# Kernel tuning notes

Measured on AMD Instinct MI355X. Metric: run time of the kernel, lower is better.

Reference implementation:

```python
import jax, jax.numpy as jnp
import numpy as np

N_HEAD = 16
HEAD_DIM = 64
EPS_RMS = 1e-6


def _rope(x, cos, sin):
    # x: [B, T, H, D]; cos/sin: [T, D//2] broadcast to [1, T, 1, D//2]
    d2 = x.shape[-1] // 2
    x1, x2 = x[..., :d2], x[..., d2:]
    c = cos[None, :, None, :]
    s = sin[None, :, None, :]
    return jnp.concatenate([x1 * c + x2 * s, -x1 * s + x2 * c], axis=-1)


def _rms_norm(x):
    return x * jax.lax.rsqrt(jnp.mean(x * x, axis=-1, keepdims=True) + EPS_RMS)


def setup_inputs() -> dict:
    key = jax.random.key(0)
    ks = jax.random.split(key, 7)
    B, T, C = 1, 4096, 1024
    x = jax.random.normal(ks[0], (B, T, C), dtype=jnp.float32)
    # realistic rotary angles
    d2 = HEAD_DIM // 2
    inv_freq = 1.0 / (10000.0 ** (np.arange(0, d2, dtype=np.float32) / d2))
    ang = np.arange(T, dtype=np.float32)[:, None] * inv_freq[None, :]
    cos = jnp.asarray(np.cos(ang), dtype=jnp.float32)
    sin = jnp.asarray(np.sin(ang), dtype=jnp.float32)
    scale = 0.02
    wq = jax.random.normal(ks[1], (C, C), dtype=jnp.float32) * scale
    wk = jax.random.normal(ks[2], (C, C), dtype=jnp.float32) * scale
    wv = jax.random.normal(ks[3], (C, C), dtype=jnp.float32) * scale
    wproj = jax.random.normal(ks[4], (C, C), dtype=jnp.float32) * scale
    return {"x": x, "cos": cos, "sin": sin, "wq": wq, "wk": wk, "wv": wv, "wproj": wproj}


def reference(x, cos, sin, wq, wk, wv, wproj):
    B, T, C = x.shape
    H, D = N_HEAD, HEAD_DIM
    # QKV projections (torch Linear: x @ W.T)
    q = (x @ wq.T).reshape(B, T, H, D)
    k = (x @ wk.T).reshape(B, T, H, D)
    v = (x @ wv.T).reshape(B, T, H, D)
    # RoPE then QK RMS-norm
    q = _rms_norm(_rope(q, cos, sin))
    k = _rms_norm(_rope(k, cos, sin))
    # [B, H, T, D]
    q = q.transpose(0, 2, 1, 3)
    k = k.transpose(0, 2, 1, 3)
    v = v.transpose(0, 2, 1, 3)
    scores = jnp.einsum('bhqd,bhkd->bhqk', q, k) * (1.0 / D ** 0.5)
    # causal mask (kv_cache is None, Tq == Tk == T)
    mask = jnp.tril(jnp.ones((T, T), dtype=bool))
    scores = jnp.where(mask[None, None, :, :], scores, -jnp.inf)
    attn = jax.nn.sigmoid(scores)  # sigmoid(-inf) == 0
    y = jnp.einsum('bhqk,bhkd->bhqd', attn, v)
    y = y / (T ** 0.5 + 1e-6)
    y = y.transpose(0, 2, 1, 3).reshape(B, T, C)
    return y @ wproj.T
```

## Files before the change

kernel.cpp:

```cpp
#include <hip/hip_runtime.h>

typedef __attribute__((ext_vector_type(8))) short bf16x8;
typedef __attribute__((ext_vector_type(4))) float f32x4;
typedef __attribute__((ext_vector_type(16))) float f32x16;

__device__ inline f32x4 mfma16(bf16x8 a, bf16x8 b, f32x4 c) {
    return __builtin_amdgcn_mfma_f32_16x16x32_bf16(a, b, c, 0, 0, 0);
}
__device__ inline f32x16 mfma32(bf16x8 a, bf16x8 b, f32x16 c) {
    return __builtin_amdgcn_mfma_f32_32x32x16_bf16(a, b, c, 0, 0, 0);
}

__device__ inline short f2bf(float f) {
    unsigned u = __builtin_bit_cast(unsigned, f);
    unsigned r = (u + 0x7fffu + ((u >> 16) & 1u)) >> 16;
    return (short)r;
}
__device__ inline float bf2f(short h) {
    unsigned u = ((unsigned)(unsigned short)h) << 16;
    return __builtin_bit_cast(float, u);
}

__device__ inline unsigned cvt_pk_bf16(float lo, float hi) {
    unsigned r;
    asm("v_cvt_pk_bf16_f32 %0, %1, %2" : "=v"(r) : "v"(lo), "v"(hi));
    return r;
}
__device__ inline void plane_swap(unsigned& a, unsigned& b) {
    asm("v_permlane32_swap_b32 %0, %1" : "+v"(a), "+v"(b));
}
__device__ inline float exp2_hw(float x) {
    float r;
    asm("v_exp_f32 %0, %1" : "=v"(r) : "v"(x));
    return r;
}

#define GAS(p) (const __attribute__((address_space(1))) void*)(p)
#define LAS(p) (__attribute__((address_space(3))) void*)(p)

#define T_SEQ 4096
#define C_DIM 1024
#define N_HEAD 16
#define HEAD_DIM 64
#define QSCALE (-0.18033688011112042f)

__global__ __launch_bounds__(256) void cast5(
    const float* __restrict__ s0, const float* __restrict__ s1,
    const float* __restrict__ s2, const float* __restrict__ s3,
    const float* __restrict__ s4,
    short* __restrict__ d0, short* __restrict__ d1, short* __restrict__ d2,
    short* __restrict__ d3, short* __restrict__ d4,
    int n0, int n1, int n2, int n3, int n4)
{
    int z = blockIdx.y;
    const float* s; short* d; int n;
    switch (z) {
        case 0: s = s0; d = d0; n = n0; break;
        case 1: s = s1; d = d1; n = n1; break;
        case 2: s = s2; d = d2; n = n2; break;
        case 3: s = s3; d = d3; n = n3; break;
        default: s = s4; d = d4; n = n4; break;
    }
    int i = (blockIdx.x * 256 + threadIdx.x) * 4;
    if (i >= n) return;
    float4 v = *(const float4*)&s[i];
    short4 o;
    o.x = f2bf(v.x); o.y = f2bf(v.y); o.z = f2bf(v.z); o.w = f2bf(v.w);
    *(short4*)&d[i] = o;
}

template<int OBF>
__global__ __launch_bounds__(256) void gemm3(
    const short* __restrict__ A,
    const short* __restrict__ B0, const short* __restrict__ B1,
    const short* __restrict__ B2,
    void* C0, void* C1, void* C2,
    int M, int N, int K)
{
    const short* B = (blockIdx.z == 0) ? B0 : ((blockIdx.z == 1) ? B1 : B2);
    void*        C = (blockIdx.z == 0) ? C0 : ((blockIdx.z == 1) ? C1 : C2);

    __shared__ alignas(16) short sA[128 * 32];
    __shared__ alignas(16) short sB[128 * 32];

    int tid  = threadIdx.x;
    int wave = tid >> 6, lane = tid & 63;
    int lhi  = lane >> 4, llo = lane & 15;
    int wr   = wave >> 1, wc = wave & 1;
    int row0 = blockIdx.x * 128, col0 = blockIdx.y * 128;

    int srow = lane >> 2;
    int scol = (lane & 3) * 8;

    f32x4 acc[4][4];
#pragma unroll
    for (int m = 0; m < 4; m++)
#pragma unroll
        for (int n = 0; n < 4; n++)
            acc[m][n] = (f32x4){0.f, 0.f, 0.f, 0.f};

    for (int k0 = 0; k0 < K; k0 += 32) {
        __syncthreads();
#pragma unroll
        for (int s2 = 0; s2 < 2; s2++) {
            int rbase = wave * 32 + s2 * 16;
            __builtin_amdgcn_global_load_lds(
                GAS(&A[(size_t)(row0 + rbase + srow) * K + k0 + scol]),
                LAS(&sA[rbase * 32]), 16, 0, 0);
            __builtin_amdgcn_global_load_lds(
                GAS(&B[(size_t)(col0 + rbase + srow) * K + k0 + scol]),
                LAS(&sB[rbase * 32]), 16, 0, 0);
        }
        __syncthreads();

        bf16x8 af[4], bfv[4];
#pragma unroll
        for (int m = 0; m < 4; m++)
            af[m] = *(const bf16x8*)&sA[(wr * 64 + m * 16 + llo) * 32 + lhi * 8];
#pragma unroll
        for (int n = 0; n < 4; n++)
            bfv[n] = *(const bf16x8*)&sB[(wc * 64 + n * 16 + llo) * 32 + lhi * 8];
#pragma unroll
        for (int m = 0; m < 4; m++)
#pragma unroll
            for (int n = 0; n < 4; n++)
                acc[m][n] = mfma16(af[m], bfv[n], acc[m][n]);
    }

#pragma unroll
    for (int m = 0; m < 4; m++)
#pragma unroll
        for (int n = 0; n < 4; n++)
#pragma unroll
            for (int r = 0; r < 4; r++) {
                int row = row0 + wr * 64 + m * 16 + lhi * 4 + r;
                int col = col0 + wc * 64 + n * 16 + llo;
                float v = acc[m][n][r];
                if (OBF) ((short*)C)[(size_t)row * N + col] = f2bf(v);
                else     ((float*)C)[(size_t)row * N + col] = v;
            }
}

__global__ __launch_bounds__(256) void rope_rms(
    const short* __restrict__ Qb, const float* __restrict__ cosT,
    const float* __restrict__ sinT, short* __restrict__ qn, float outscale)
{
    int idx = blockIdx.x * 4 + (threadIdx.x >> 6);
    int t = idx >> 4, h = idx & 15;
    int d = threadIdx.x & 63;

    float v = bf2f(Qb[t * C_DIM + h * HEAD_DIM + d]);
    int d2 = d & 31;
    float c = cosT[t * 32 + d2], s = sinT[t * 32 + d2];
    float other = __shfl_xor(v, 32);
    float r = (d < 32) ? (v * c + other * s) : (v * c - other * s);

    float sq = r * r;
#pragma unroll
    for (int off = 32; off >= 1; off >>= 1) sq += __shfl_xor(sq, off);
    float inv = rsqrtf(sq * (1.0f / 64.0f) + 1e-6f);

    qn[((size_t)h * T_SEQ + t) * HEAD_DIM + d] = f2bf(r * inv * outscale);
}

__global__ __launch_bounds__(256) void vtrans(
    const short* __restrict__ Vb, short* __restrict__ vt)
{
    __shared__ short sT[64 * 65];
    int h = blockIdx.y, tb = blockIdx.x;
    int tid = threadIdx.x;
    const float inv64 = 1.0f / (64.0f + 1e-6f);
#pragma unroll
    for (int i = 0; i < 16; i++) {
        int linear = i * 256 + tid;
        int r = linear >> 6, c = linear & 63;
        float v = bf2f(Vb[(size_t)(tb * 64 + r) * C_DIM + h * HEAD_DIM + c]) * inv64;
        sT[c * 65 + r] = f2bf(v);
    }
    __syncthreads();
#pragma unroll
    for (int i = 0; i < 16; i++) {
        int linear = i * 256 + tid;
        int dd = linear >> 6, tt = linear & 63;
        vt[((size_t)(h * HEAD_DIM + dd)) * T_SEQ + tb * 64 + tt] = sT[dd * 65 + tt];
    }
}


#define STAGE(s_, bf_) do {                                                      \
    int kb_ = (s_) * 64;                                                         \
    int r0_ = wv * 8 + (lane >> 3);                                              \
    int ss_ = (lane & 7) ^ (lane >> 3);                                          \
    __builtin_amdgcn_global_load_lds(                                            \
        GAS(Kh + (size_t)(kb_ + r0_) * HEAD_DIM + ss_ * 8),                      \
        LAS(Smem + (bf_) * 8192 + wv * 1024), 16, 0, 0);                         \
    __builtin_amdgcn_global_load_lds(                                            \
        GAS(Vh + (size_t)r0_ * T_SEQ + kb_ + ss_ * 8),                           \
        LAS(Smem + 16384 + (bf_) * 8192 + wv * 1024), 16, 0, 0);                 \
} while (0)

__global__ __launch_bounds__(512, 4) void attn5(
    const short* __restrict__ qn, const short* __restrict__ kn,
    const short* __restrict__ vt, short* __restrict__ yb)
{
    __shared__ alignas(16) char Smem[32768];

    int id  = blockIdx.x;
    int idx = id >> 3;
    int h   = (id & 7) * 2 + (idx & 1);
    int sq  = idx >> 1;
    int t   = (sq < 16) ? (31 - sq) : (sq - 16);
    int ns  = 2 * t + 2;

    int tid = threadIdx.x, wv = tid >> 6, lane = tid & 63;
    int lo = lane & 31, hi = lane >> 5;
    int band = wv & 3, tm = wv >> 2;

    const short* Qh = qn + (size_t)h * T_SEQ * HEAD_DIM;
    const short* Kh = kn + (size_t)h * T_SEQ * HEAD_DIM;
    const short* Vh = vt + (size_t)h * HEAD_DIM * T_SEQ;

    int q0 = t * 128;
    int qrow  = q0 + band * 32 + lo;
    int qmaxw = q0 + band * 32 + 31;

    const short* Qr = &Qh[(size_t)qrow * HEAD_DIM + hi * 8];
    bf16x8 qf0 = *(const bf16x8*)&Qr[0];
    bf16x8 qf1 = *(const bf16x8*)&Qr[16];
    bf16x8 qf2 = *(const bf16x8*)&Qr[32];
    bf16x8 qf3 = *(const bf16x8*)&Qr[48];

    f32x16 yac0, yac1;
#pragma unroll
    for (int r = 0; r < 16; r++) { yac0[r] = 0.f; yac1[r] = 0.f; }

    unsigned swz   = (unsigned)((lo & 7) << 4);
    unsigned krow  = (unsigned)((tm * 32 + lo) * 128);
    unsigned vbase = 16384u;

    STAGE(0, 0);
    int buf = 0;
    for (int s = 0; s < ns; s++) {
        if (s + 1 < ns) {
            STAGE(s + 1, buf ^ 1);
            asm volatile("s_waitcnt vmcnt(2)" ::: "memory");
        } else {
            asm volatile("s_waitcnt vmcnt(0)" ::: "memory");
        }
        __builtin_amdgcn_s_barrier();

        int kb0 = s * 64 + tm * 32;
        if (kb0 <= qmaxw) {
            const char* KB = Smem + buf * 8192;
            const char* VB = Smem + vbase + buf * 8192;
            bf16x8 kf0 = *(const bf16x8*)(KB + krow + ((0u * 32 + hi * 16) ^ swz));
            bf16x8 kf1 = *(const bf16x8*)(KB + krow + ((1u * 32 + hi * 16) ^ swz));
            bf16x8 kf2 = *(const bf16x8*)(KB + krow + ((2u * 32 + hi * 16) ^ swz));
            bf16x8 kf3 = *(const bf16x8*)(KB + krow + ((3u * 32 + hi * 16) ^ swz));
            unsigned v0r = (unsigned)((0 * 32 + lo) * 128);
            unsigned v1r = (unsigned)((1 * 32 + lo) * 128);
            unsigned vswz = (unsigned)((lo & 7) << 4);
            bf16x8 vf00 = *(const bf16x8*)(VB + v0r + (((unsigned)(tm * 64 + 0 * 32 + hi * 16)) ^ vswz));
            bf16x8 vf01 = *(const bf16x8*)(VB + v0r + (((unsigned)(tm * 64 + 1 * 32 + hi * 16)) ^ vswz));
            bf16x8 vf10 = *(const bf16x8*)(VB + v1r + (((unsigned)(tm * 64 + 0 * 32 + hi * 16)) ^ vswz));
            bf16x8 vf11 = *(const bf16x8*)(VB + v1r + (((unsigned)(tm * 64 + 1 * 32 + hi * 16)) ^ vswz));

            f32x16 sv;
#pragma unroll
            for (int r = 0; r < 16; r++) sv[r] = 0.f;
            __builtin_amdgcn_s_setprio(1);
            sv = mfma32(kf0, qf0, sv);
            sv = mfma32(kf1, qf1, sv);
            sv = mfma32(kf2, qf2, sv);
            sv = mfma32(kf3, qf3, sv);
            __builtin_amdgcn_s_setprio(0);

            if (kb0 + 31 > q0 + band * 32) {
#pragma unroll
                for (int r = 0; r < 16; r++) {
                    int kvg = kb0 + (r & 3) + 8 * (r >> 2) + 4 * hi;
                    float pv = __builtin_amdgcn_rcpf(1.f + exp2_hw(sv[r]));
                    sv[r] = (kvg <= qrow) ? pv : 0.f;
                }
            } else {
#pragma unroll
                for (int r = 0; r < 16; r++)
                    sv[r] = __builtin_amdgcn_rcpf(1.f + exp2_hw(sv[r]));
            }

#pragma unroll
            for (int k2 = 0; k2 < 2; k2++) {
                unsigned wA = cvt_pk_bf16(sv[8 * k2 + 0], sv[8 * k2 + 1]);
                unsigned wC = cvt_pk_bf16(sv[8 * k2 + 2], sv[8 * k2 + 3]);
                unsigned wB = cvt_pk_bf16(sv[8 * k2 + 4], sv[8 * k2 + 5]);
                unsigned wD = cvt_pk_bf16(sv[8 * k2 + 6], sv[8 * k2 + 7]);
                plane_swap(wA, wB);
                plane_swap(wC, wD);
                union { unsigned u[4]; bf16x8 v; } pw;
                pw.u[0] = wA; pw.u[1] = wC; pw.u[2] = wB; pw.u[3] = wD;
                __builtin_amdgcn_s_setprio(1);
                yac0 = mfma32(pw.v, k2 ? vf01 : vf00, yac0);
                yac1 = mfma32(pw.v, k2 ? vf11 : vf10, yac1);
                __builtin_amdgcn_s_setprio(0);
            }
        }
        asm volatile("" ::: "memory");
        __builtin_amdgcn_s_barrier();
        buf ^= 1;
    }

    __syncthreads();
    float* Yred = (float*)Smem;
    if (tm == 1) {
#pragma unroll
        for (int d = 0; d < 2; d++)
#pragma unroll
            for (int r = 0; r < 16; r++) {
                int crow = (r & 3) + 8 * (r >> 2) + 4 * hi;
                Yred[(band * 32 + crow) * 64 + d * 32 + lo] = d ? yac1[r] : yac0[r];
            }
    }
    __syncthreads();
    if (tm == 0) {
#pragma unroll
        for (int d = 0; d < 2; d++)
#pragma unroll
            for (int r = 0; r < 16; r++) {
                int crow = (r & 3) + 8 * (r >> 2) + 4 * hi;
                float v = (d ? yac1[r] : yac0[r]) + Yred[(band * 32 + crow) * 64 + d * 32 + lo];
                yb[(size_t)(q0 + band * 32 + crow) * C_DIM + h * HEAD_DIM + d * 32 + lo] = f2bf(v);
            }
    }
}

extern "C" void kernel_launch(void* const* d_in, const int* in_sizes, int n_in,
                              void* d_out, int out_size, void* d_ws, size_t ws_size,
                              hipStream_t stream)
{
    const float* x    = (const float*)d_in[0];
    const float* cosT = (const float*)d_in[1];
    const float* sinT = (const float*)d_in[2];
    const float* wq   = (const float*)d_in[3];
    const float* wk   = (const float*)d_in[4];
    const float* wv   = (const float*)d_in[5];
    const float* wp   = (const float*)d_in[6];

    char* ws = (char*)d_ws;
    const size_t MB = 1024 * 1024;
    short* xb  = (short*)(ws + 0);
    short* wqb = (short*)(ws + 8  * MB);
    short* wkb = (short*)(ws + 10 * MB);
    short* wvb = (short*)(ws + 12 * MB);
    short* wpb = (short*)(ws + 14 * MB);
    short* Qb  = (short*)(ws + 16 * MB);
    short* Kb  = (short*)(ws + 24 * MB);
    short* Vb  = (short*)(ws + 32 * MB);
    short* qnb = (short*)(ws + 40 * MB);
    short* knb = (short*)(ws + 48 * MB);
    short* vtb = (short*)(ws + 56 * MB);
    short* yb  = (short*)(ws + 64 * MB);

    cast5<<<dim3(4096, 5, 1), 256, 0, stream>>>(
        x, wq, wk, wv, wp, xb, wqb, wkb, wvb, wpb,
        T_SEQ * C_DIM, C_DIM * C_DIM, C_DIM * C_DIM, C_DIM * C_DIM, C_DIM * C_DIM);

    gemm3<1><<<dim3(32, 8, 3), 256, 0, stream>>>(
        xb, wqb, wkb, wvb, (void*)Qb, (void*)Kb, (void*)Vb, T_SEQ, C_DIM, C_DIM);

    rope_rms<<<16384, 256, 0, stream>>>(Qb, cosT, sinT, qnb, QSCALE);
    rope_rms<<<16384, 256, 0, stream>>>(Kb, cosT, sinT, knb, 1.0f);

    vtrans<<<dim3(64, 16, 1), 256, 0, stream>>>(Vb, vtb);

    attn5<<<512, 512, 0, stream>>>(qnb, knb, vtb, yb);

    gemm3<0><<<dim3(32, 8, 1), 256, 0, stream>>>(
        yb, wpb, wpb, wpb, d_out, d_out, d_out, T_SEQ, C_DIM, C_DIM);
}
```

Baseline: 159.4 us.

## Fuse Q/K rope-norm into vectorized kernel and halve attention query tile

The two per-element rope_rms launches become one rope2 kernel that handles both Q and K. Each thread in it processes 8 contiguous bf16 values with vector loads and stores and reduces over an 8-lane shuffle group. The attention kernel moves from 128-query blocks of 8 waves to 64-query blocks of 4 waves, doubling the grid to 1024 blocks with a reordered causal schedule for load balance. Each wave now issues four LDS-direct loads per stage, and LDS offsets are precomputed outside the loop. The aim is to cut launch overhead and narrow memory traffic for rope, and to improve occupancy and balance in attention, at the cost of reloading K/V per query block more often.

```diff
diff --git a/kernel.cpp b/kernel.cpp
--- a/kernel.cpp
+++ b/kernel.cpp
@@ -141,26 +141,54 @@
             }
 }
 
-__global__ __launch_bounds__(256) void rope_rms(
-    const short* __restrict__ Qb, const float* __restrict__ cosT,
-    const float* __restrict__ sinT, short* __restrict__ qn, float outscale)
-{
-    int idx = blockIdx.x * 4 + (threadIdx.x >> 6);
-    int t = idx >> 4, h = idx & 15;
-    int d = threadIdx.x & 63;
-
-    float v = bf2f(Qb[t * C_DIM + h * HEAD_DIM + d]);
-    int d2 = d & 31;
-    float c = cosT[t * 32 + d2], s = sinT[t * 32 + d2];
-    float other = __shfl_xor(v, 32);
-    float r = (d < 32) ? (v * c + other * s) : (v * c - other * s);
-
-    float sq = r * r;
-#pragma unroll
-    for (int off = 32; off >= 1; off >>= 1) sq += __shfl_xor(sq, off);
-    float inv = rsqrtf(sq * (1.0f / 64.0f) + 1e-6f);
-
-    qn[((size_t)h * T_SEQ + t) * HEAD_DIM + d] = f2bf(r * inv * outscale);
+__global__ __launch_bounds__(256) void rope2(
+    const short* __restrict__ Qb, const short* __restrict__ Kb,
+    const float* __restrict__ cosT, const float* __restrict__ sinT,
+    short* __restrict__ qnb, short* __restrict__ knb)
+{
+    int z = blockIdx.y;
+    const short* src = z ? Kb : Qb;
+    short* dst = z ? knb : qnb;
+    float osc = z ? 1.0f : QSCALE;
+
+    int rowg = blockIdx.x * 32 + (threadIdx.x >> 3);
+    int t = rowg >> 4, h = rowg & 15;
+    int j = threadIdx.x & 7;
+
+    bf16x8 v8 = *(const bf16x8*)&src[(size_t)t * C_DIM + h * HEAD_DIM + j * 8];
+    float f[8], o[8];
+#pragma unroll
+    for (int i = 0; i < 8; i++) f[i] = bf2f(v8[i]);
+#pragma unroll
+    for (int i = 0; i < 8; i++) o[i] = __shfl_xor(f[i], 4);
+
+    const float* cp = &cosT[t * 32 + (j & 3) * 8];
+    const float* sp = &sinT[t * 32 + (j & 3) * 8];
+    float4 c0 = *(const float4*)&cp[0], c1 = *(const float4*)&cp[4];
+    float4 s0 = *(const float4*)&sp[0], s1 = *(const float4*)&sp[4];
+    float cc[8] = {c0.x, c0.y, c0.z, c0.w, c1.x, c1.y, c1.z, c1.w};
+    float ss[8] = {s0.x, s0.y, s0.z, s0.w, s1.x, s1.y, s1.z, s1.w};
+
+    float r[8];
+    if (j < 4) {
+#pragma unroll
+        for (int i = 0; i < 8; i++) r[i] = f[i] * cc[i] + o[i] * ss[i];
+    } else {
+#pragma unroll
+        for (int i = 0; i < 8; i++) r[i] = f[i] * cc[i] - o[i] * ss[i];
+    }
+
+    float sq = 0.f;
+#pragma unroll
+    for (int i = 0; i < 8; i++) sq += r[i] * r[i];
+#pragma unroll
+    for (int off = 1; off <= 4; off <<= 1) sq += __shfl_xor(sq, off);
+    float inv = rsqrtf(sq * (1.0f / 64.0f) + 1e-6f) * osc;
+
+    bf16x8 out;
+#pragma unroll
+    for (int i = 0; i < 8; i++) out[i] = f2bf(r[i] * inv);
+    *(bf16x8*)&dst[((size_t)h * T_SEQ + t) * HEAD_DIM + j * 8] = out;
 }
 
 __global__ __launch_bounds__(256) void vtrans(
@@ -187,40 +215,46 @@
 }
 
 
-#define STAGE(s_, bf_) do {                                                      \
+#define STAGE6(s_, bf_) do {                                                     \
     int kb_ = (s_) * 64;                                                         \
-    int r0_ = wv * 8 + (lane >> 3);                                              \
-    int ss_ = (lane & 7) ^ (lane >> 3);                                          \
+    int r_  = lane >> 3;                                                         \
+    int ss_ = (lane & 7) ^ r_;                                                   \
     __builtin_amdgcn_global_load_lds(                                            \
-        GAS(Kh + (size_t)(kb_ + r0_) * HEAD_DIM + ss_ * 8),                      \
-        LAS(Smem + (bf_) * 8192 + wv * 1024), 16, 0, 0);                         \
+        GAS(Kh + (size_t)(kb_ + wv * 16 + r_) * HEAD_DIM + ss_ * 8),             \
+        LAS(Smem + (bf_) * 8192 + (wv * 16) * 128), 16, 0, 0);                   \
     __builtin_amdgcn_global_load_lds(                                            \
-        GAS(Vh + (size_t)r0_ * T_SEQ + kb_ + ss_ * 8),                           \
-        LAS(Smem + 16384 + (bf_) * 8192 + wv * 1024), 16, 0, 0);                 \
+        GAS(Kh + (size_t)(kb_ + wv * 16 + 8 + r_) * HEAD_DIM + ss_ * 8),         \
+        LAS(Smem + (bf_) * 8192 + (wv * 16 + 8) * 128), 16, 0, 0);               \
+    __builtin_amdgcn_global_load_lds(                                            \
+        GAS(Vh + (size_t)(wv * 16 + r_) * T_SEQ + kb_ + ss_ * 8),                \
+        LAS(Smem + 16384 + (bf_) * 8192 + (wv * 16) * 128), 16, 0, 0);           \
+    __builtin_amdgcn_global_load_lds(                                            \
+        GAS(Vh + (size_t)(wv * 16 + 8 + r_) * T_SEQ + kb_ + ss_ * 8),            \
+        LAS(Smem + 16384 + (bf_) * 8192 + (wv * 16 + 8) * 128), 16, 0, 0);       \
 } while (0)
 
-__global__ __launch_bounds__(512, 4) void attn5(
+__global__ __launch_bounds__(256, 4) void attn6(
     const short* __restrict__ qn, const short* __restrict__ kn,
     const short* __restrict__ vt, short* __restrict__ yb)
 {
     __shared__ alignas(16) char Smem[32768];
 
-    int id  = blockIdx.x;
-    int idx = id >> 3;
-    int h   = (id & 7) * 2 + (idx & 1);
-    int sq  = idx >> 1;
-    int t   = (sq < 16) ? (31 - sq) : (sq - 16);
-    int ns  = 2 * t + 2;
+    int id = blockIdx.x;
+    int h  = id & 15;
+    int g  = id >> 4;
+    int t  = (g < 16) ? (63 - g) : (g < 32) ? (g - 16)
+           : (g < 48) ? (79 - g) : (g - 32);
+    int ns = t + 1;
 
     int tid = threadIdx.x, wv = tid >> 6, lane = tid & 63;
     int lo = lane & 31, hi = lane >> 5;
-    int band = wv & 3, tm = wv >> 2;
+    int band = wv & 1, tm = wv >> 1;
 
     const short* Qh = qn + (size_t)h * T_SEQ * HEAD_DIM;
     const short* Kh = kn + (size_t)h * T_SEQ * HEAD_DIM;
     const short* Vh = vt + (size_t)h * HEAD_DIM * T_SEQ;
 
-    int q0 = t * 128;
+    int q0 = t * 64;
     int qrow  = q0 + band * 32 + lo;
     int qmaxw = q0 + band * 32 + 31;
 
@@ -230,20 +264,33 @@
     bf16x8 qf2 = *(const bf16x8*)&Qr[32];
     bf16x8 qf3 = *(const bf16x8*)&Qr[48];
 
+    f32x16 zed;
+#pragma unroll
+    for (int r = 0; r < 16; r++) zed[r] = 0.f;
+
     f32x16 yac0, yac1;
 #pragma unroll
     for (int r = 0; r < 16; r++) { yac0[r] = 0.f; yac1[r] = 0.f; }
 
-    unsigned swz   = (unsigned)((lo & 7) << 4);
-    unsigned krow  = (unsigned)((tm * 32 + lo) * 128);
-    unsigned vbase = 16384u;
-
-    STAGE(0, 0);
+    unsigned sw   = (unsigned)((lo & 7) << 4);
+    unsigned krow = (unsigned)((tm * 32 + lo) * 128);
+    unsigned ko0 = krow + ((0u * 32 + hi * 16) ^ sw);
+    unsigned ko1 = krow + ((1u * 32 + hi * 16) ^ sw);
+    unsigned ko2 = krow + ((2u * 32 + hi * 16) ^ sw);
+    unsigned ko3 = krow + ((3u * 32 + hi * 16) ^ sw);
+    unsigned vrow0 = (unsigned)(lo * 128)        + 16384u;
+    unsigned vrow1 = (unsigned)((32 + lo) * 128) + 16384u;
+    unsigned vo00 = vrow0 + (((unsigned)(tm * 64 + 0 * 32 + hi * 16)) ^ sw);
+    unsigned vo01 = vrow0 + (((unsigned)(tm * 64 + 1 * 32 + hi * 16)) ^ sw);
+    unsigned vo10 = vrow1 + (((unsigned)(tm * 64 + 0 * 32 + hi * 16)) ^ sw);
+    unsigned vo11 = vrow1 + (((unsigned)(tm * 64 + 1 * 32 + hi * 16)) ^ sw);
+
+    STAGE6(0, 0);
     int buf = 0;
     for (int s = 0; s < ns; s++) {
         if (s + 1 < ns) {
-            STAGE(s + 1, buf ^ 1);
-            asm volatile("s_waitcnt vmcnt(2)" ::: "memory");
+            STAGE6(s + 1, buf ^ 1);
+            asm volatile("s_waitcnt vmcnt(4)" ::: "memory");
         } else {
             asm volatile("s_waitcnt vmcnt(0)" ::: "memory");
         }
@@ -251,25 +298,19 @@
 
         int kb0 = s * 64 + tm * 32;
         if (kb0 <= qmaxw) {
-            const char* KB = Smem + buf * 8192;
-            const char* VB = Smem + vbase + buf * 8192;
-            bf16x8 kf0 = *(const bf16x8*)(KB + krow + ((0u * 32 + hi * 16) ^ swz));
-            bf16x8 kf1 = *(const bf16x8*)(KB + krow + ((1u * 32 + hi * 16) ^ swz));
-            bf16x8 kf2 = *(const bf16x8*)(KB + krow + ((2u * 32 + hi * 16) ^ swz));
-            bf16x8 kf3 = *(const bf16x8*)(KB + krow + ((3u * 32 + hi * 16) ^ swz));
-            unsigned v0r = (unsigned)((0 * 32 + lo) * 128);
-            unsigned v1r = (unsigned)((1 * 32 + lo) * 128);
-            unsigned vswz = (unsigned)((lo & 7) << 4);
-            bf16x8 vf00 = *(const bf16x8*)(VB + v0r + (((unsigned)(tm * 64 + 0 * 32 + hi * 16)) ^ vswz));
-            bf16x8 vf01 = *(const bf16x8*)(VB + v0r + (((unsigned)(tm * 64 + 1 * 32 + hi * 16)) ^ vswz));
-            bf16x8 vf10 = *(const bf16x8*)(VB + v1r + (((unsigned)(tm * 64 + 0 * 32 + hi * 16)) ^ vswz));
-            bf16x8 vf11 = *(const bf16x8*)(VB + v1r + (((unsigned)(tm * 64 + 1 * 32 + hi * 16)) ^ vswz));
+            const char* B_ = Smem + (buf << 13);
+            bf16x8 kf0 = *(const bf16x8*)(B_ + ko0);
+            bf16x8 kf1 = *(const bf16x8*)(B_ + ko1);
+            bf16x8 kf2 = *(const bf16x8*)(B_ + ko2);
+            bf16x8 kf3 = *(const bf16x8*)(B_ + ko3);
+            bf16x8 vf00 = *(const bf16x8*)(B_ + vo00);
+            bf16x8 vf01 = *(const bf16x8*)(B_ + vo01);
+            bf16x8 vf10 = *(const bf16x8*)(B_ + vo10);
+            bf16x8 vf11 = *(const bf16x8*)(B_ + vo11);
 
             f32x16 sv;
-#pragma unroll
-            for (int r = 0; r < 16; r++) sv[r] = 0.f;
             __builtin_amdgcn_s_setprio(1);
-            sv = mfma32(kf0, qf0, sv);
+            sv = mfma32(kf0, qf0, zed);
             sv = mfma32(kf1, qf1, sv);
             sv = mfma32(kf2, qf2, sv);
             sv = mfma32(kf3, qf3, sv);
@@ -367,12 +408,11 @@
     gemm3<1><<<dim3(32, 8, 3), 256, 0, stream>>>(
         xb, wqb, wkb, wvb, (void*)Qb, (void*)Kb, (void*)Vb, T_SEQ, C_DIM, C_DIM);
 
-    rope_rms<<<16384, 256, 0, stream>>>(Qb, cosT, sinT, qnb, QSCALE);
-    rope_rms<<<16384, 256, 0, stream>>>(Kb, cosT, sinT, knb, 1.0f);
+    rope2<<<dim3(2048, 2, 1), 256, 0, stream>>>(Qb, Kb, cosT, sinT, qnb, knb);
 
     vtrans<<<dim3(64, 16, 1), 256, 0, stream>>>(Vb, vtb);
 
-    attn5<<<512, 512, 0, stream>>>(qnb, knb, vtb, yb);
+    attn6<<<1024, 256, 0, stream>>>(qnb, knb, vtb, yb);
 
     gemm3<0><<<dim3(32, 8, 1), 256, 0, stream>>>(
         yb, wpb, wpb, wpb, d_out, d_out, d_out, T_SEQ, C_DIM, C_DIM);
```

New measurement: 142.3 us. 1.12x faster.
